# Performance work log

Hardware: AMD Instinct MI355X
Metric: run time of the kernel (lower is better)

The kernel has to match this reference:

```python
import jax, jax.numpy as jnp
import numpy as np

P = 512       # protein_dim
D = 512       # drug_dim
N = 2000      # neighbors per layer
E = 300000    # binding edges per layer
ND = 100000   # total drugs
BASELINE = 6.0
LN_EPS = 1e-5


def setup_inputs() -> dict:
    key = jax.random.key(0)
    ks = jax.random.split(key, 24)
    inp = {
        "target_features": jax.random.normal(ks[0], (P,), jnp.float32),
        "form_features": jax.random.normal(ks[1], (N, P), jnp.float32),
        "role_features": jax.random.normal(ks[2], (N, P), jnp.float32),
        "form_neighbors": jnp.arange(N, dtype=jnp.int64) if jax.config.jax_enable_x64 else jnp.arange(N, dtype=jnp.int32),
        "role_neighbors": jnp.arange(N, dtype=jnp.int32),
        "form_binds_ei": jax.random.randint(ks[3], (2, E), 0, N, jnp.int32),
        "form_binds_y": jax.random.uniform(ks[4], (E,), jnp.float32) * 8.0 + 2.0,
        "role_binds_ei": jax.random.randint(ks[5], (2, E), 0, N, jnp.int32),
        "role_binds_y": jax.random.uniform(ks[6], (E,), jnp.float32) * 8.0 + 2.0,
        "drug_features": jax.random.normal(ks[7], (ND, D), jnp.float32),
    }
    inp["form_neighbors"] = jnp.arange(N, dtype=jnp.int32)
    attn_in = P * 2 + 16
    s1 = 1.0 / np.sqrt(attn_in)
    s2 = 1.0 / np.sqrt(64)
    sd = 1.0 / np.sqrt(D)
    sp = 1.0 / np.sqrt(P)
    inp["layer_emb"] = jax.random.normal(ks[8], (2, 16), jnp.float32)
    inp["W1"] = jax.random.uniform(ks[9], (attn_in, 64), jnp.float32, -s1, s1)
    inp["b1"] = jax.random.uniform(ks[10], (64,), jnp.float32, -s1, s1)
    inp["W2"] = jax.random.uniform(ks[11], (64, 1), jnp.float32, -s2, s2)
    inp["b2"] = jax.random.uniform(ks[12], (1,), jnp.float32, -s2, s2)
    inp["Wi1"] = jax.random.uniform(ks[13], (D, P), jnp.float32, -sd, sd)
    inp["bi1"] = jax.random.uniform(ks[14], (P,), jnp.float32, -sd, sd)
    inp["prelu_alpha"] = jnp.array(0.25, jnp.float32)
    inp["Wi2"] = jax.random.uniform(ks[15], (P, P), jnp.float32, -sp, sp)
    inp["bi2"] = jax.random.uniform(ks[16], (P,), jnp.float32, -sp, sp)
    inp["ln_gamma"] = jnp.ones((P,), jnp.float32)
    inp["ln_beta"] = jnp.zeros((P,), jnp.float32)
    return inp


def _pref_vectors(neighbor_ids, ei, y, drug_features):
    # Vectorized form of the per-neighbor masked gather-sum:
    # for each edge, find its neighbor slot (neighbor_ids is sorted);
    # edges whose src id is not a neighbor get zero weight.
    n = neighbor_ids.shape[0]
    pos = jnp.clip(jnp.searchsorted(neighbor_ids, ei[0]), 0, n - 1)
    valid = neighbor_ids[pos] == ei[0]
    w = jnp.where(valid, y - BASELINE, 0.0)              # [E]
    contrib = drug_features[ei[1]] * w[:, None]          # [E, D] gather (memory-bound)
    return jax.ops.segment_sum(contrib, pos, num_segments=n)  # [N, D]


def _attention(z_target, z_neighbors, l_vec, W1, b1, W2, b2):
    n = z_neighbors.shape[0]
    inp = jnp.concatenate(
        [jnp.broadcast_to(z_target, (n, z_target.shape[0])),
         z_neighbors,
         jnp.broadcast_to(l_vec, (n, l_vec.shape[0]))], axis=-1)  # [N, 2P+16]
    h = inp @ W1 + b1
    h = jnp.where(h > 0, h, 0.2 * h)  # LeakyReLU(0.2)
    return h @ W2 + b2                # [N, 1]


def reference(target_features, form_features, role_features, form_neighbors,
              role_neighbors, form_binds_ei, form_binds_y, role_binds_ei,
              role_binds_y, drug_features, layer_emb, W1, b1, W2, b2,
              Wi1, bi1, prelu_alpha, Wi2, bi2, ln_gamma, ln_beta):
    form_msgs = _pref_vectors(form_neighbors, form_binds_ei, form_binds_y, drug_features)
    role_msgs = _pref_vectors(role_neighbors, role_binds_ei, role_binds_y, drug_features)

    form_attn = _attention(target_features, form_features, layer_emb[0], W1, b1, W2, b2)
    role_attn = _attention(target_features, role_features, layer_emb[1], W1, b1, W2, b2)

    all_msgs = jnp.concatenate([form_msgs, role_msgs], axis=0)   # [2N, D]
    all_attn = jnp.concatenate([form_attn, role_attn], axis=0)   # [2N, 1]
    attn_weights = jax.nn.softmax(all_attn, axis=0)
    v_prior = jnp.sum(attn_weights * all_msgs, axis=0)           # [D]

    h = v_prior @ Wi1 + bi1
    h = jnp.where(h > 0, h, prelu_alpha * h)  # PReLU
    v = h @ Wi2 + bi2                          # [P]

    x = target_features + v
    mu = jnp.mean(x)
    var = jnp.mean(jnp.square(x - mu))
    z_refined = (x - mu) / jnp.sqrt(var + LN_EPS) * ln_gamma + ln_beta
    return (z_refined, form_msgs, role_msgs)
```

## Files before the change

kernel.cpp:

```cpp
#include <hip/hip_runtime.h>
#include <math.h>

static constexpr int PD = 512;
static constexpr float BASEV = 6.0f;
static constexpr int CAP = 320;

__global__ __launch_bounds__(256) void front_kernel(
    const int* __restrict__ ei_f, const float* __restrict__ y_f,
    const int* __restrict__ ei_r, const float* __restrict__ y_r,
    const int* __restrict__ nb_f, const int* __restrict__ nb_r,
    const float* __restrict__ target, const float* __restrict__ formF,
    const float* __restrict__ roleF, const float* __restrict__ lemb,
    const float* __restrict__ W1, const float* __restrict__ b1,
    const float* __restrict__ W2, const float* __restrict__ b2,
    int N, int E, int AB, int EBf,
    int* __restrict__ cnt, int2* __restrict__ bins,
    float* __restrict__ logits) {
    __shared__ int snb[2048];
    int b = blockIdx.x;
    if (b >= AB) {
        int b2 = b - AB;
        bool role = b2 >= EBf;
        const int* nb = role ? nb_r : nb_f;
        const int* ei = role ? ei_r : ei_f;
        const float* yy = role ? y_r : y_f;
        bool lds_ok = (N <= 2048);
        if (lds_ok) {
            for (int i = threadIdx.x; i < N; i += 256) snb[i] = nb[i];
            __syncthreads();
        }
        int base = (role ? b2 - EBf : b2) * 1024;
        int K = 32 - __clz(N);
        int v[4], lo[4], hi[4], e[4];
#pragma unroll
        for (int r = 0; r < 4; r++) {
            e[r] = base + threadIdx.x + r * 256;
            bool a = e[r] < E;
            v[r] = a ? ei[e[r]] : 0;
            lo[r] = 0; hi[r] = a ? N : 0;
        }
        if (lds_ok) {
            for (int it = 0; it < K; it++) {
#pragma unroll
                for (int r = 0; r < 4; r++) {
                    if (lo[r] < hi[r]) {
                        int mid = (lo[r] + hi[r]) >> 1;
                        if (snb[mid] < v[r]) lo[r] = mid + 1; else hi[r] = mid;
                    }
                }
            }
        } else {
            for (int it = 0; it < K; it++) {
#pragma unroll
                for (int r = 0; r < 4; r++) {
                    if (lo[r] < hi[r]) {
                        int mid = (lo[r] + hi[r]) >> 1;
                        if (nb[mid] < v[r]) lo[r] = mid + 1; else hi[r] = mid;
                    }
                }
            }
        }
#pragma unroll
        for (int r = 0; r < 4; r++) {
            if (e[r] >= E) continue;
            int pos = lo[r] < N ? lo[r] : N - 1;
            int nbp = lds_ok ? snb[pos] : nb[pos];
            if (nbp != v[r]) continue;
            int s = role ? N + pos : pos;
            float w = yy[e[r]] - BASEV;
            int slot = atomicAdd(&cnt[s], 1);
            if (slot < CAP) bins[(size_t)s * CAP + slot] = make_int2(ei[E + e[r]], __float_as_int(w));
        }
    } else {
        int wave = threadIdx.x >> 6, lane = threadIdx.x & 63;
        int r0 = (b * 4 + wave) * 4;
        int nseg = 2 * N;
        if (r0 >= nseg) return;
        const float* W1t = W1 + lane;
        float c = b1[lane];
        const float4* t4 = (const float4*)target;
        for (int p = 0; p < PD; p += 4) {
            float4 tv = t4[p >> 2];
            c += tv.x * W1t[(size_t)(p + 0) * 64] + tv.y * W1t[(size_t)(p + 1) * 64]
               + tv.z * W1t[(size_t)(p + 2) * 64] + tv.w * W1t[(size_t)(p + 3) * 64];
        }
        float c0 = c, c1 = c;
        for (int q = 0; q < 16; q++) {
            float wq = W1t[(size_t)(2 * PD + q) * 64];
            c0 += lemb[q] * wq;
            c1 += lemb[16 + q] * wq;
        }
        int nrows = nseg - r0; if (nrows > 4) nrows = 4;
        const float* z[4];
        float hA[4], hB[4];
#pragma unroll
        for (int r = 0; r < 4; r++) {
            int rr = r0 + (r < nrows ? r : 0);
            bool rl = rr >= N;
            z[r] = rl ? roleF + (size_t)(rr - N) * PD : formF + (size_t)rr * PD;
            hA[r] = rl ? c1 : c0;
            hB[r] = 0.f;
        }
        const float* W1z = W1 + (size_t)PD * 64 + lane;
        for (int p = 0; p < PD; p += 4) {
            float w0 = W1z[(size_t)(p + 0) * 64], w1 = W1z[(size_t)(p + 1) * 64];
            float w2 = W1z[(size_t)(p + 2) * 64], w3 = W1z[(size_t)(p + 3) * 64];
#pragma unroll
            for (int r = 0; r < 4; r++) {
                float4 zv = *(const float4*)(z[r] + p);
                hA[r] += zv.x * w0 + zv.y * w1;
                hB[r] += zv.z * w2 + zv.w * w3;
            }
        }
        float w2l = W2[lane];
#pragma unroll
        for (int r = 0; r < 4; r++) {
            float hh = hA[r] + hB[r];
            hh = hh > 0.f ? hh : 0.2f * hh;
            float vv = hh * w2l;
#pragma unroll
            for (int off = 32; off > 0; off >>= 1) vv += __shfl_down(vv, off, 64);
            if (lane == 0 && r < nrows) logits[r0 + r] = vv + b2[0];
        }
    }
}

__global__ __launch_bounds__(128) void accum_kernel(const int* __restrict__ cnt,
                                                    const int2* __restrict__ bins,
                                                    const float* __restrict__ drug,
                                                    float* __restrict__ msgs) {
    int b = blockIdx.x;
    int t = threadIdx.x;
    int n = cnt[b]; n = n < CAP ? n : CAP;
    const int2* bb = bins + (size_t)b * CAP;
    float4 acc = make_float4(0.f, 0.f, 0.f, 0.f);
    int k = 0;
    for (; k + 7 < n; k += 8) {
        int2 e0 = bb[k + 0], e1 = bb[k + 1], e2 = bb[k + 2], e3 = bb[k + 3];
        int2 e4 = bb[k + 4], e5 = bb[k + 5], e6 = bb[k + 6], e7 = bb[k + 7];
        float4 d0 = ((const float4*)(drug + (size_t)e0.x * PD))[t];
        float4 d1 = ((const float4*)(drug + (size_t)e1.x * PD))[t];
        float4 d2 = ((const float4*)(drug + (size_t)e2.x * PD))[t];
        float4 d3 = ((const float4*)(drug + (size_t)e3.x * PD))[t];
        float4 d4 = ((const float4*)(drug + (size_t)e4.x * PD))[t];
        float4 d5 = ((const float4*)(drug + (size_t)e5.x * PD))[t];
        float4 d6 = ((const float4*)(drug + (size_t)e6.x * PD))[t];
        float4 d7 = ((const float4*)(drug + (size_t)e7.x * PD))[t];
        float w0 = __int_as_float(e0.y), w1 = __int_as_float(e1.y);
        float w2 = __int_as_float(e2.y), w3 = __int_as_float(e3.y);
        float w4 = __int_as_float(e4.y), w5 = __int_as_float(e5.y);
        float w6 = __int_as_float(e6.y), w7 = __int_as_float(e7.y);
        acc.x += w0 * d0.x; acc.y += w0 * d0.y; acc.z += w0 * d0.z; acc.w += w0 * d0.w;
        acc.x += w1 * d1.x; acc.y += w1 * d1.y; acc.z += w1 * d1.z; acc.w += w1 * d1.w;
        acc.x += w2 * d2.x; acc.y += w2 * d2.y; acc.z += w2 * d2.z; acc.w += w2 * d2.w;
        acc.x += w3 * d3.x; acc.y += w3 * d3.y; acc.z += w3 * d3.z; acc.w += w3 * d3.w;
        acc.x += w4 * d4.x; acc.y += w4 * d4.y; acc.z += w4 * d4.z; acc.w += w4 * d4.w;
        acc.x += w5 * d5.x; acc.y += w5 * d5.y; acc.z += w5 * d5.z; acc.w += w5 * d5.w;
        acc.x += w6 * d6.x; acc.y += w6 * d6.y; acc.z += w6 * d6.z; acc.w += w6 * d6.w;
        acc.x += w7 * d7.x; acc.y += w7 * d7.y; acc.z += w7 * d7.z; acc.w += w7 * d7.w;
    }
    for (; k < n; k++) {
        int2 e0 = bb[k];
        float w0 = __int_as_float(e0.y);
        float4 d0 = ((const float4*)(drug + (size_t)e0.x * PD))[t];
        acc.x += w0 * d0.x; acc.y += w0 * d0.y; acc.z += w0 * d0.z; acc.w += w0 * d0.w;
    }
    ((float4*)(msgs + (size_t)b * PD))[t] = acc;
}

__global__ __launch_bounds__(128) void vprior_kernel(const float* __restrict__ logits,
                                                     const float* __restrict__ msgs,
                                                     int nseg, float* __restrict__ v_prior) {
    __shared__ float red[128];
    int t = threadIdx.x;
    float m = -1e30f;
    for (int s = t; s < nseg; s += 128) m = fmaxf(m, logits[s]);
    red[t] = m; __syncthreads();
    for (int o = 64; o > 0; o >>= 1) { if (t < o) red[t] = fmaxf(red[t], red[t + o]); __syncthreads(); }
    m = red[0]; __syncthreads();
    float sum = 0.f;
    for (int s = t; s < nseg; s += 128) sum += expf(logits[s] - m);
    red[t] = sum; __syncthreads();
    for (int o = 64; o > 0; o >>= 1) { if (t < o) red[t] += red[t + o]; __syncthreads(); }
    float inv = 1.f / red[0];

    float4 acc = make_float4(0.f, 0.f, 0.f, 0.f);
    for (int s = blockIdx.x; s < nseg; s += gridDim.x) {
        float w = expf(logits[s] - m) * inv;
        float4 d = ((const float4*)(msgs + (size_t)s * PD))[t];
        acc.x += w * d.x; acc.y += w * d.y; acc.z += w * d.z; acc.w += w * d.w;
    }
    atomicAdd(&v_prior[4 * t + 0], acc.x);
    atomicAdd(&v_prior[4 * t + 1], acc.y);
    atomicAdd(&v_prior[4 * t + 2], acc.z);
    atomicAdd(&v_prior[4 * t + 3], acc.w);
}

__global__ __launch_bounds__(256) void mv1_kernel(const float* __restrict__ v_prior,
                                                  const float* __restrict__ Wi1,
                                                  float* __restrict__ h) {
    int b = blockIdx.x;
    int t = threadIdx.x;
    float2 acc = make_float2(0.f, 0.f);
    int d0 = b * 16;
    for (int d = d0; d < d0 + 16; d++) {
        float vd = v_prior[d];
        float2 w = ((const float2*)(Wi1 + (size_t)d * PD))[t];
        acc.x += vd * w.x; acc.y += vd * w.y;
    }
    atomicAdd(&h[2 * t + 0], acc.x);
    atomicAdd(&h[2 * t + 1], acc.y);
}

__global__ __launch_bounds__(256) void mv2_kernel(const float* __restrict__ h,
                                                  const float* __restrict__ bi1,
                                                  const float* __restrict__ alpha_p,
                                                  const float* __restrict__ Wi2,
                                                  float* __restrict__ v) {
    int b = blockIdx.x;
    int t = threadIdx.x;
    float alpha = alpha_p[0];
    float2 acc = make_float2(0.f, 0.f);
    int q0 = b * 16;
    for (int q = q0; q < q0 + 16; q++) {
        float hq = h[q] + bi1[q];
        hq = hq > 0.f ? hq : alpha * hq;
        float2 w = ((const float2*)(Wi2 + (size_t)q * PD))[t];
        acc.x += hq * w.x; acc.y += hq * w.y;
    }
    atomicAdd(&v[2 * t + 0], acc.x);
    atomicAdd(&v[2 * t + 1], acc.y);
}

__global__ __launch_bounds__(512) void final_kernel(const float* __restrict__ target,
                                                    const float* __restrict__ v,
                                                    const float* __restrict__ bi2,
                                                    const float* __restrict__ gamma,
                                                    const float* __restrict__ beta,
                                                    float* __restrict__ out) {
    __shared__ float red[512];
    int t = threadIdx.x;
    float x = target[t] + v[t] + bi2[t];
    red[t] = x; __syncthreads();
    for (int o = 256; o > 0; o >>= 1) { if (t < o) red[t] += red[t + o]; __syncthreads(); }
    float mu = red[0] * (1.f / 512.f);
    __syncthreads();
    float dx = x - mu;
    red[t] = dx * dx; __syncthreads();
    for (int o = 256; o > 0; o >>= 1) { if (t < o) red[t] += red[t + o]; __syncthreads(); }
    float var = red[0] * (1.f / 512.f);
    out[t] = dx * (1.f / sqrtf(var + 1e-5f)) * gamma[t] + beta[t];
}

extern "C" void kernel_launch(void* const* d_in, const int* in_sizes, int n_in,
                              void* d_out, int out_size, void* d_ws, size_t ws_size,
                              hipStream_t stream) {
    const float* target = (const float*)d_in[0];
    const float* formF  = (const float*)d_in[1];
    const float* roleF  = (const float*)d_in[2];
    const int*   nb_f   = (const int*)d_in[3];
    const int*   nb_r   = (const int*)d_in[4];
    const int*   ei_f   = (const int*)d_in[5];
    const float* y_f    = (const float*)d_in[6];
    const int*   ei_r   = (const int*)d_in[7];
    const float* y_r    = (const float*)d_in[8];
    const float* drug   = (const float*)d_in[9];
    const float* lemb   = (const float*)d_in[10];
    const float* W1     = (const float*)d_in[11];
    const float* b1     = (const float*)d_in[12];
    const float* W2     = (const float*)d_in[13];
    const float* b2     = (const float*)d_in[14];
    const float* Wi1    = (const float*)d_in[15];
    const float* bi1    = (const float*)d_in[16];
    const float* alpha  = (const float*)d_in[17];
    const float* Wi2    = (const float*)d_in[18];
    const float* bi2    = (const float*)d_in[19];
    const float* gamma  = (const float*)d_in[20];
    const float* beta   = (const float*)d_in[21];

    int N = in_sizes[3];
    int E = in_sizes[5] / 2;
    int nseg = 2 * N;

    int* ws = (int*)d_ws;
    int*   cnt     = ws + 0;
    float* v_prior = (float*)(ws + 4096);
    float* hbuf    = (float*)(ws + 4608);
    float* vbuf    = (float*)(ws + 5120);
    float* logits  = (float*)(ws + 5632);
    int2*  bins    = (int2*)(ws + 9728);

    float* out  = (float*)d_out;
    float* msgs = out + PD;

    hipMemsetAsync(ws, 0, 5632 * sizeof(int), stream);

    int AB  = (nseg + 15) / 16;
    int EBf = (E + 1023) / 1024;
    front_kernel<<<AB + 2 * EBf, 256, 0, stream>>>(ei_f, y_f, ei_r, y_r, nb_f, nb_r,
                                                   target, formF, roleF, lemb,
                                                   W1, b1, W2, b2, N, E, AB, EBf,
                                                   cnt, bins, logits);
    accum_kernel<<<nseg, 128, 0, stream>>>(cnt, bins, drug, msgs);
    vprior_kernel<<<64, 128, 0, stream>>>(logits, msgs, nseg, v_prior);
    mv1_kernel<<<32, 256, 0, stream>>>(v_prior, Wi1, hbuf);
    mv2_kernel<<<32, 256, 0, stream>>>(hbuf, bi1, alpha, Wi2, vbuf);
    final_kernel<<<1, 512, 0, stream>>>(target, vbuf, bi2, gamma, beta, out);
}
```

Baseline: 456.1 us.

## Split attention logits to one row per wave with block-shared target projection

The attention branch of front_kernel now gives each wave a single feature row instead of four, so it launches four times as many attention blocks. Each block computes the shared target/layer-embedding projection once, splitting it across its four waves and combining the partials through shared memory, instead of every wave recomputing it alone. This is meant to raise parallelism and shorten the serial per-wave critical path. The cost is more blocks, which repeat the target projection and W1 loads block-wide and add two __syncthreads.

```diff
diff --git a/kernel.cpp b/kernel.cpp
--- a/kernel.cpp
+++ b/kernel.cpp
@@ -72,56 +72,54 @@
             if (slot < CAP) bins[(size_t)s * CAP + slot] = make_int2(ei[E + e[r]], __float_as_int(w));
         }
     } else {
+        float* spart = (float*)snb;
+        float* sc0 = spart + 256;
+        float* sc1 = spart + 320;
+        int jj = threadIdx.x & 63, ck = threadIdx.x >> 6;
+        const float* Wc = W1 + jj;
+        float tp = 0.f;
+        int p0 = ck * 128;
+        for (int p = p0; p < p0 + 128; p += 4) {
+            float4 tv = *(const float4*)(target + p);
+            tp += tv.x * Wc[(size_t)(p + 0) * 64] + tv.y * Wc[(size_t)(p + 1) * 64]
+                + tv.z * Wc[(size_t)(p + 2) * 64] + tv.w * Wc[(size_t)(p + 3) * 64];
+        }
+        spart[ck * 64 + jj] = tp;
+        __syncthreads();
+        if (ck == 0) {
+            float c = b1[jj] + spart[jj] + spart[64 + jj] + spart[128 + jj] + spart[192 + jj];
+            float c0 = c, c1 = c;
+            for (int q = 0; q < 16; q++) {
+                float wq = Wc[(size_t)(2 * PD + q) * 64];
+                c0 += lemb[q] * wq;
+                c1 += lemb[16 + q] * wq;
+            }
+            sc0[jj] = c0; sc1[jj] = c1;
+        }
+        __syncthreads();
         int wave = threadIdx.x >> 6, lane = threadIdx.x & 63;
-        int r0 = (b * 4 + wave) * 4;
+        int rr = b * 4 + wave;
         int nseg = 2 * N;
-        if (r0 >= nseg) return;
-        const float* W1t = W1 + lane;
-        float c = b1[lane];
-        const float4* t4 = (const float4*)target;
-        for (int p = 0; p < PD; p += 4) {
-            float4 tv = t4[p >> 2];
-            c += tv.x * W1t[(size_t)(p + 0) * 64] + tv.y * W1t[(size_t)(p + 1) * 64]
-               + tv.z * W1t[(size_t)(p + 2) * 64] + tv.w * W1t[(size_t)(p + 3) * 64];
-        }
-        float c0 = c, c1 = c;
-        for (int q = 0; q < 16; q++) {
-            float wq = W1t[(size_t)(2 * PD + q) * 64];
-            c0 += lemb[q] * wq;
-            c1 += lemb[16 + q] * wq;
-        }
-        int nrows = nseg - r0; if (nrows > 4) nrows = 4;
-        const float* z[4];
-        float hA[4], hB[4];
-#pragma unroll
-        for (int r = 0; r < 4; r++) {
-            int rr = r0 + (r < nrows ? r : 0);
-            bool rl = rr >= N;
-            z[r] = rl ? roleF + (size_t)(rr - N) * PD : formF + (size_t)rr * PD;
-            hA[r] = rl ? c1 : c0;
-            hB[r] = 0.f;
-        }
-        const float* W1z = W1 + (size_t)PD * 64 + lane;
-        for (int p = 0; p < PD; p += 4) {
-            float w0 = W1z[(size_t)(p + 0) * 64], w1 = W1z[(size_t)(p + 1) * 64];
-            float w2 = W1z[(size_t)(p + 2) * 64], w3 = W1z[(size_t)(p + 3) * 64];
-#pragma unroll
-            for (int r = 0; r < 4; r++) {
-                float4 zv = *(const float4*)(z[r] + p);
-                hA[r] += zv.x * w0 + zv.y * w1;
-                hB[r] += zv.z * w2 + zv.w * w3;
-            }
-        }
-        float w2l = W2[lane];
-#pragma unroll
-        for (int r = 0; r < 4; r++) {
-            float hh = hA[r] + hB[r];
-            hh = hh > 0.f ? hh : 0.2f * hh;
-            float vv = hh * w2l;
-#pragma unroll
-            for (int off = 32; off > 0; off >>= 1) vv += __shfl_down(vv, off, 64);
-            if (lane == 0 && r < nrows) logits[r0 + r] = vv + b2[0];
-        }
+        if (rr >= nseg) return;
+        bool rl = rr >= N;
+        const float* z = rl ? roleF + (size_t)(rr - N) * PD : formF + (size_t)rr * PD;
+        const float* Wz = W1 + (size_t)PD * 64 + lane;
+        float hA = rl ? sc1[lane] : sc0[lane];
+        float hB = 0.f, hC = 0.f, hD = 0.f;
+        for (int p = 0; p < PD; p += 8) {
+            float4 z0 = *(const float4*)(z + p);
+            float4 z1 = *(const float4*)(z + p + 4);
+            hA += z0.x * Wz[(size_t)(p + 0) * 64] + z0.y * Wz[(size_t)(p + 1) * 64];
+            hB += z0.z * Wz[(size_t)(p + 2) * 64] + z0.w * Wz[(size_t)(p + 3) * 64];
+            hC += z1.x * Wz[(size_t)(p + 4) * 64] + z1.y * Wz[(size_t)(p + 5) * 64];
+            hD += z1.z * Wz[(size_t)(p + 6) * 64] + z1.w * Wz[(size_t)(p + 7) * 64];
+        }
+        float hh = (hA + hB) + (hC + hD);
+        hh = hh > 0.f ? hh : 0.2f * hh;
+        float vv = hh * W2[lane];
+#pragma unroll
+        for (int off = 32; off > 0; off >>= 1) vv += __shfl_down(vv, off, 64);
+        if (lane == 0) logits[rr] = vv + b2[0];
     }
 }
 
@@ -295,7 +293,7 @@
 
     hipMemsetAsync(ws, 0, 5632 * sizeof(int), stream);
 
-    int AB  = (nseg + 15) / 16;
+    int AB  = (nseg + 3) / 4;
     int EBf = (E + 1023) / 1024;
     front_kernel<<<AB + 2 * EBf, 256, 0, stream>>>(ei_f, y_f, ei_r, y_r, nb_f, nb_r,
                                                    target, formF, roleF, lemb,
```

Result: no change. 452.8 us (-0.7%).
